# Optimization experiments

Measured on AMD Instinct MI355X. Metric: run time of the kernel, lower is better.

## Reference

```python
import jax, jax.numpy as jnp
import numpy as np

K = 3
K2 = K * K
PAD = (K - 1) // 2
DECAY_RATE = 4.0
REL_THRESHOLD = 0.3
EPS = 1e-8


def _deform_sample(depth, offset):
    """Deformable bilinear gather equivalent to the fixed-identity-weight
    ModulatedDeformConv2d (mask=1, bias=0). Returns [B, K2, H, W]."""
    B, _, H, W = depth.shape
    d = depth[:, 0]  # [B, H, W]
    dt = depth.dtype
    # mmcv offset layout: channel 2*i = dy, 2*i+1 = dx for kernel point i
    off = offset.reshape(B, K2, 2, H, W)
    off_y, off_x = off[:, :, 0], off[:, :, 1]          # [B, K2, H, W]
    ky = (jnp.arange(K2) // K - PAD).astype(dt)        # [K2]
    kx = (jnp.arange(K2) % K - PAD).astype(dt)
    ys = jnp.arange(H, dtype=dt)
    xs = jnp.arange(W, dtype=dt)
    # sampling locations: p = base_pixel + kernel_offset + learned_offset
    py = off_y + ys[None, None, :, None] + ky[None, :, None, None]  # [B,K2,H,W]
    px = off_x + xs[None, None, None, :] + kx[None, :, None, None]
    y0 = jnp.floor(py)
    x0 = jnp.floor(px)
    wy = py - y0  # bilinear weights
    wx = px - x0
    y0i = y0.astype(jnp.int32)
    x0i = x0.astype(jnp.int32)

    def gather(iy, ix):
        # zero-padded gather (matches mmcv out-of-bounds handling)
        valid = (iy >= 0) & (iy < H) & (ix >= 0) & (ix < W)
        iyc = jnp.clip(iy, 0, H - 1)
        ixc = jnp.clip(ix, 0, W - 1)
        vals = jax.vmap(lambda img, a, b: img[a, b])(d, iyc, ixc)  # [B,K2,H,W]
        return jnp.where(valid, vals, jnp.zeros((), dt))

    v00 = gather(y0i, x0i)
    v01 = gather(y0i, x0i + 1)
    v10 = gather(y0i + 1, x0i)
    v11 = gather(y0i + 1, x0i + 1)
    return (v00 * (1 - wy) * (1 - wx) + v01 * (1 - wy) * wx
            + v10 * wy * (1 - wx) + v11 * wy * wx)


def setup_inputs() -> dict:
    key = jax.random.key(0)
    k1, k2 = jax.random.split(key)
    B, H, W = 8, 480, 640
    depth = jax.random.uniform(k1, (B, 1, H, W), dtype=jnp.float32)
    offset = jax.random.normal(k2, (B, 2 * K2, H, W), dtype=jnp.float32)
    return {"depth": depth, "offset": offset}


def reference(depth, offset):
    sampled = _deform_sample(depth, offset)           # [B, K2, H, W]
    center = sampled[:, K2 // 2: K2 // 2 + 1]         # [B, 1, H, W]
    depth_diff = jnp.abs(sampled - center)
    # normalize_mode == 'threshold' (default path)
    relative_diff = depth_diff / (center + EPS)
    within = relative_diff <= REL_THRESHOLD
    affinity = jnp.exp(-DECAY_RATE * (depth_diff - center * REL_THRESHOLD))
    return jnp.where(within, jnp.ones_like(affinity), affinity)
```

## Files before the change

### kernel.cpp

```cpp
#include <hip/hip_runtime.h>

constexpr int KK = 3;
constexpr int K2 = 9;
constexpr int PADC = 1;
constexpr float DECAY = 4.0f;
constexpr float RELT = 0.3f;
constexpr float EPSV = 1e-8f;
constexpr int H = 480;
constexpr int W = 640;
constexpr int HW = H * W;

constexpr int TH = 8;
constexpr int TW = 64;
constexpr int PADT = 8;
constexpr int LR = TH + 2 * PADT;
constexpr int LC = TW + 2 * PADT;
constexpr int LSTRIDE = LC + 1;
constexpr int NSTAGE = LR * LC;

__device__ __forceinline__ float dsample(const float* __restrict__ img, int iy, int ix) {
    bool valid = (iy >= 0) & (iy < H) & (ix >= 0) & (ix < W);
    int iyc = min(max(iy, 0), H - 1);
    int ixc = min(max(ix, 0), W - 1);
    float v = img[iyc * W + ixc];
    return valid ? v : 0.0f;
}

__global__ __launch_bounds__(256) void affinity_kernel(
    const float* __restrict__ depth,
    const float* __restrict__ offset,
    float* __restrict__ out)
{
    const int bx0 = blockIdx.x * TW;
    const int by0 = blockIdx.y * TH;
    const int b   = blockIdx.z;
    const int t   = threadIdx.x;

    __shared__ float tile[LR * LSTRIDE];

    const float* __restrict__ dimg = depth + (size_t)b * HW;

#pragma unroll
    for (int i = 0; i < (NSTAGE + 255) / 256; ++i) {
        int idx = t + i * 256;
        if (idx < NSTAGE) {
            int r = idx / LC;
            int c = idx - r * LC;
            int yi = by0 - PADT + r;
            int xi = bx0 - PADT + c;
            float v = 0.0f;
            if ((unsigned)yi < (unsigned)H && (unsigned)xi < (unsigned)W)
                v = dimg[yi * W + xi];
            tile[r * LSTRIDE + c] = v;
        }
    }
    __syncthreads();

    const int c  = t & 63;
    const int r0 = t >> 6;

#pragma unroll
    for (int pi = 0; pi < 2; ++pi) {
        const int r = r0 + pi * 4;
        const int y = by0 + r;
        const int x = bx0 + c;

        const size_t base = ((size_t)b * 2 * K2) * HW + (size_t)y * W + x;
        float oy[K2], ox[K2];
#pragma unroll
        for (int k = 0; k < K2; ++k) {
            oy[k] = offset[base + (size_t)(2 * k) * HW];
            ox[k] = offset[base + (size_t)(2 * k + 1) * HW];
        }

        float s[K2];
#pragma unroll
        for (int k = 0; k < K2; ++k) {
            float pyt = oy[k] + (float)(r + PADT + k / KK - PADC);
            float pxt = ox[k] + (float)(c + PADT + k % KK - PADC);
            float y0f = floorf(pyt);
            float x0f = floorf(pxt);
            float wy = pyt - y0f;
            float wx = pxt - x0f;
            int y0 = (int)y0f;
            int x0 = (int)x0f;
            float v00, v01, v10, v11;
            if ((unsigned)y0 < (unsigned)(LR - 1) && (unsigned)x0 < (unsigned)(LC - 1)) {
                int a = y0 * LSTRIDE + x0;
                v00 = tile[a];
                v01 = tile[a + 1];
                v10 = tile[a + LSTRIDE];
                v11 = tile[a + LSTRIDE + 1];
            } else {
                int gy = y0 + by0 - PADT;
                int gx = x0 + bx0 - PADT;
                v00 = dsample(dimg, gy, gx);
                v01 = dsample(dimg, gy, gx + 1);
                v10 = dsample(dimg, gy + 1, gx);
                v11 = dsample(dimg, gy + 1, gx + 1);
            }
            float wy1 = 1.0f - wy;
            float wx1 = 1.0f - wx;
            s[k] = v00 * wy1 * wx1 + v01 * wy1 * wx + v10 * wy * wx1 + v11 * wy * wx;
        }

        const float cv  = s[K2 / 2];
        const float thr = RELT * (cv + EPSV);
        const float cr  = RELT * cv;

        const size_t obase = ((size_t)b * K2) * HW + (size_t)y * W + x;
#pragma unroll
        for (int k = 0; k < K2; ++k) {
            float diff = fabsf(s[k] - cv);
            float aff = __expf(-DECAY * (diff - cr));
            out[obase + (size_t)k * HW] = (diff <= thr) ? 1.0f : aff;
        }
    }
}

extern "C" void kernel_launch(void* const* d_in, const int* in_sizes, int n_in,
                              void* d_out, int out_size, void* d_ws, size_t ws_size,
                              hipStream_t stream) {
    const float* depth = (const float*)d_in[0];
    const float* offset = (const float*)d_in[1];
    float* out = (float*)d_out;

    int B = in_sizes[0] / HW;
    dim3 grid(W / TW, H / TH, B);
    affinity_kernel<<<grid, 256, 0, stream>>>(depth, offset, out);
}
```

Before: 55.30 us.

## Vectorize offset loads and output stores, 4 pixels per thread, taller tile

Each thread now handles 4 adjacent pixels in one row and loads the offsets with float4 vector loads. Outputs are written with float4 nontemporal stores, and the centre channel is stored as a constant 1 without computing it. The tile height doubles to 16 rows, which cuts the fraction of halo reloads, and the staging loop drops its bounds check because NSTAGE is now a multiple of 256. In exchange, each thread does more work and uses more registers, and the grid has half as many blocks.

```diff
diff --git a/kernel.cpp b/kernel.cpp
--- a/kernel.cpp
+++ b/kernel.cpp
@@ -10,7 +10,9 @@
 constexpr int W = 640;
 constexpr int HW = H * W;
 
-constexpr int TH = 8;
+typedef float f32x4 __attribute__((ext_vector_type(4)));
+
+constexpr int TH = 16;
 constexpr int TW = 64;
 constexpr int PADT = 8;
 constexpr int LR = TH + 2 * PADT;
@@ -24,6 +26,42 @@
     int ixc = min(max(ix, 0), W - 1);
     float v = img[iyc * W + ixc];
     return valid ? v : 0.0f;
+}
+
+__device__ __forceinline__ void tap4(const float* __restrict__ tile,
+                                     const float* __restrict__ dimg,
+                                     int by0, int bx0, int r, int col,
+                                     f32x4 oy, f32x4 ox, int ky, int kx,
+                                     float* s4) {
+#pragma unroll
+    for (int j = 0; j < 4; ++j) {
+        float pyt = oy[j] + (float)(r + PADT + ky);
+        float pxt = ox[j] + (float)(col + j + PADT + kx);
+        float y0f = floorf(pyt);
+        float x0f = floorf(pxt);
+        float wy = pyt - y0f;
+        float wx = pxt - x0f;
+        int y0 = (int)y0f;
+        int x0 = (int)x0f;
+        float v00, v01, v10, v11;
+        if ((unsigned)y0 < (unsigned)(LR - 1) && (unsigned)x0 < (unsigned)(LC - 1)) {
+            int a = y0 * LSTRIDE + x0;
+            v00 = tile[a];
+            v01 = tile[a + 1];
+            v10 = tile[a + LSTRIDE];
+            v11 = tile[a + LSTRIDE + 1];
+        } else {
+            int gy = y0 + by0 - PADT;
+            int gx = x0 + bx0 - PADT;
+            v00 = dsample(dimg, gy, gx);
+            v01 = dsample(dimg, gy, gx + 1);
+            v10 = dsample(dimg, gy + 1, gx);
+            v11 = dsample(dimg, gy + 1, gx + 1);
+        }
+        float wy1 = 1.0f - wy;
+        float wx1 = 1.0f - wx;
+        s4[j] = v00 * wy1 * wx1 + v01 * wy1 * wx + v10 * wy * wx1 + v11 * wy * wx;
+    }
 }
 
 __global__ __launch_bounds__(256) void affinity_kernel(
@@ -41,80 +79,62 @@
     const float* __restrict__ dimg = depth + (size_t)b * HW;
 
 #pragma unroll
-    for (int i = 0; i < (NSTAGE + 255) / 256; ++i) {
+    for (int i = 0; i < NSTAGE / 256; ++i) {
         int idx = t + i * 256;
-        if (idx < NSTAGE) {
-            int r = idx / LC;
-            int c = idx - r * LC;
-            int yi = by0 - PADT + r;
-            int xi = bx0 - PADT + c;
-            float v = 0.0f;
-            if ((unsigned)yi < (unsigned)H && (unsigned)xi < (unsigned)W)
-                v = dimg[yi * W + xi];
-            tile[r * LSTRIDE + c] = v;
-        }
+        int r = idx / LC;
+        int c = idx - r * LC;
+        int yi = by0 - PADT + r;
+        int xi = bx0 - PADT + c;
+        float v = 0.0f;
+        if ((unsigned)yi < (unsigned)H && (unsigned)xi < (unsigned)W)
+            v = dimg[yi * W + xi];
+        tile[r * LSTRIDE + c] = v;
     }
     __syncthreads();
 
-    const int c  = t & 63;
-    const int r0 = t >> 6;
+    const int col = (t & 15) * 4;
+    const int r   = t >> 4;
+    const int y   = by0 + r;
+    const int x   = bx0 + col;
+
+    const size_t obase = ((size_t)b * 2 * K2) * HW + (size_t)y * W + x;
+    const float* __restrict__ offp = offset + obase;
+
+    float c4[4];
+    {
+        f32x4 oy = *reinterpret_cast<const f32x4*>(offp + (size_t)8 * HW);
+        f32x4 ox = *reinterpret_cast<const f32x4*>(offp + (size_t)9 * HW);
+        tap4(tile, dimg, by0, bx0, r, col, oy, ox, 0, 0, c4);
+    }
+    float thr[4], cr[4];
+#pragma unroll
+    for (int j = 0; j < 4; ++j) {
+        thr[j] = RELT * (c4[j] + EPSV);
+        cr[j]  = RELT * c4[j];
+    }
+
+    float* __restrict__ outp = out + ((size_t)b * K2) * HW + (size_t)y * W + x;
+
+    {
+        f32x4 ones = {1.0f, 1.0f, 1.0f, 1.0f};
+        __builtin_nontemporal_store(ones, reinterpret_cast<f32x4*>(outp + (size_t)4 * HW));
+    }
 
 #pragma unroll
-    for (int pi = 0; pi < 2; ++pi) {
-        const int r = r0 + pi * 4;
-        const int y = by0 + r;
-        const int x = bx0 + c;
-
-        const size_t base = ((size_t)b * 2 * K2) * HW + (size_t)y * W + x;
-        float oy[K2], ox[K2];
+    for (int k = 0; k < K2; ++k) {
+        if (k == 4) continue;
+        f32x4 oy = *reinterpret_cast<const f32x4*>(offp + (size_t)(2 * k) * HW);
+        f32x4 ox = *reinterpret_cast<const f32x4*>(offp + (size_t)(2 * k + 1) * HW);
+        float s4[4];
+        tap4(tile, dimg, by0, bx0, r, col, oy, ox, k / KK - PADC, k % KK - PADC, s4);
+        f32x4 vals;
 #pragma unroll
-        for (int k = 0; k < K2; ++k) {
-            oy[k] = offset[base + (size_t)(2 * k) * HW];
-            ox[k] = offset[base + (size_t)(2 * k + 1) * HW];
+        for (int j = 0; j < 4; ++j) {
+            float diff = fabsf(s4[j] - c4[j]);
+            float aff = __expf(-DECAY * (diff - cr[j]));
+            vals[j] = (diff <= thr[j]) ? 1.0f : aff;
         }
-
-        float s[K2];
-#pragma unroll
-        for (int k = 0; k < K2; ++k) {
-            float pyt = oy[k] + (float)(r + PADT + k / KK - PADC);
-            float pxt = ox[k] + (float)(c + PADT + k % KK - PADC);
-            float y0f = floorf(pyt);
-            float x0f = floorf(pxt);
-            float wy = pyt - y0f;
-            float wx = pxt - x0f;
-            int y0 = (int)y0f;
-            int x0 = (int)x0f;
-            float v00, v01, v10, v11;
-            if ((unsigned)y0 < (unsigned)(LR - 1) && (unsigned)x0 < (unsigned)(LC - 1)) {
-                int a = y0 * LSTRIDE + x0;
-                v00 = tile[a];
-                v01 = tile[a + 1];
-                v10 = tile[a + LSTRIDE];
-                v11 = tile[a + LSTRIDE + 1];
-            } else {
-                int gy = y0 + by0 - PADT;
-                int gx = x0 + bx0 - PADT;
-                v00 = dsample(dimg, gy, gx);
-                v01 = dsample(dimg, gy, gx + 1);
-                v10 = dsample(dimg, gy + 1, gx);
-                v11 = dsample(dimg, gy + 1, gx + 1);
-            }
-            float wy1 = 1.0f - wy;
-            float wx1 = 1.0f - wx;
-            s[k] = v00 * wy1 * wx1 + v01 * wy1 * wx + v10 * wy * wx1 + v11 * wy * wx;
-        }
-
-        const float cv  = s[K2 / 2];
-        const float thr = RELT * (cv + EPSV);
-        const float cr  = RELT * cv;
-
-        const size_t obase = ((size_t)b * K2) * HW + (size_t)y * W + x;
-#pragma unroll
-        for (int k = 0; k < K2; ++k) {
-            float diff = fabsf(s[k] - cv);
-            float aff = __expf(-DECAY * (diff - cr));
-            out[obase + (size_t)k * HW] = (diff <= thr) ? 1.0f : aff;
-        }
+        __builtin_nontemporal_store(vals, reinterpret_cast<f32x4*>(outp + (size_t)k * HW));
     }
 }
 
```

After: 49.65 us. 10.2% less time.
